# Kernel tuning notes

Measured on AMD Instinct MI355X. Metric: run time of the kernel, lower is better.

The kernel has to match this reference:

```python
import jax, jax.numpy as jnp
import numpy as np

NUM_HEADS = 12
EPS = 1e-6


def setup_inputs() -> dict:
    key = jax.random.key(0)
    k1, k2, k3, k4 = jax.random.split(key, 4)
    N, B, D = 1025, 8, 768
    x = jax.random.normal(k1, (N, B, D), dtype=jnp.float32)
    # torch nn.Linear weights: [out_features, in_features]
    w_qkv = jax.random.normal(k2, (3 * D, D), dtype=jnp.float32) * (D ** -0.5)
    w_proj = jax.random.normal(k3, (D, D), dtype=jnp.float32) * (D ** -0.5)
    b_proj = jax.random.normal(k4, (D,), dtype=jnp.float32) * 0.01
    return {"x": x, "w_qkv": w_qkv, "w_proj": w_proj, "b_proj": b_proj}


def reference(x, w_qkv, w_proj, b_proj):
    N, B, D = x.shape
    H = NUM_HEADS
    hd = D // H
    scale = hd ** -0.5
    scale_vv = scale * 1.0  # scale_multiplier = 1.0

    xb = jnp.transpose(x, (1, 0, 2))  # [B, N, D]
    qkv = xb @ w_qkv.T  # [B, N, 3D]
    qkv = qkv.reshape(B, N, 3, H, hd).transpose(2, 0, 3, 1, 4)  # [3, B, H, N, hd]
    q, k, v = qkv[0], qkv[1], qkv[2]

    # QK path: only row 0 of out_ori survives the masking, compute just that row
    scores0 = jnp.einsum('bhqd,bhkd->bhqk', q[:, :, :1], k) * scale  # [B,H,1,N]
    attn0 = jax.nn.softmax(scores0, axis=-1)
    out0 = jnp.einsum('bhqk,bhkd->bhqd', attn0, v)  # [B,H,1,hd]

    # VV cosine path: only rows 1: survive
    vn = v / jnp.maximum(jnp.linalg.norm(v, axis=-1, keepdims=True), EPS)
    scores_vv = jnp.einsum('bhqd,bhkd->bhqk', vn[:, :, 1:], vn) * scale_vv  # [B,H,N-1,N]
    attn_vv = jax.nn.softmax(scores_vv, axis=-1)
    out_vv = jnp.einsum('bhqk,bhkd->bhqd', attn_vv, v)  # [B,H,N-1,hd]

    out = jnp.concatenate([out0, out_vv], axis=2)  # [B,H,N,hd]
    out = out.transpose(0, 2, 1, 3).reshape(B, N, D)
    out = out @ w_proj.T + b_proj
    return jnp.transpose(out, (1, 0, 2))  # [N, B, D]
```

## Files before the change

### kernel.cpp

```cpp
#include <hip/hip_runtime.h>

typedef unsigned short u16;
typedef unsigned int   u32;
typedef __attribute__((ext_vector_type(8))) short short8;
typedef __attribute__((ext_vector_type(4))) float f32x4;

#define AS1 __attribute__((address_space(1)))
#define AS3 __attribute__((address_space(3)))

#define NSEQ  1025
#define BB    8
#define DD    768
#define HH    12
#define MROWS 8200
#define MPAD  8320
#define KPAD  1088

__device__ __forceinline__ void gl2lds16(const void* g, void* l) {
  __builtin_amdgcn_global_load_lds((const AS1 u32*)g, (AS3 u32*)l, 16, 0, 0);
}
__device__ __forceinline__ u16 f2bf(float f) {
  u32 u = __float_as_uint(f);
  return (u16)((u + 0x7FFFu + ((u >> 16) & 1u)) >> 16);
}
__device__ __forceinline__ float bf2f(u16 u) { return __uint_as_float(((u32)u) << 16); }

__global__ __launch_bounds__(256) void prep(const float* __restrict__ x,
                                            const float* __restrict__ wqkv,
                                            const float* __restrict__ wproj,
                                            u16* __restrict__ xb,
                                            u16* __restrict__ wkv,
                                            u16* __restrict__ wpj) {
  const int XB_G  = MPAD * 192;
  const int WKV_G = 1536 * 192;
  const int WPJ_G = 768 * 192;
  int g = blockIdx.x * 256 + threadIdx.x;
  float4 v;
  u16* dst;
  size_t di;
  if (g < XB_G) {
    int m = g / 192, e4 = g - m * 192;
    if (m < MROWS) {
      int bb = m / NSEQ, ns = m - bb * NSEQ;
      v = ((const float4*)x)[(size_t)(ns * BB + bb) * 192 + e4];
    } else {
      v.x = v.y = v.z = v.w = 0.f;
    }
    dst = xb; di = (size_t)g;
  } else if (g < XB_G + WKV_G) {
    int r = g - XB_G;
    v = ((const float4*)wqkv)[(size_t)147456 + r];
    dst = wkv; di = (size_t)r;
  } else if (g < XB_G + WKV_G + WPJ_G) {
    int r = g - XB_G - WKV_G;
    v = ((const float4*)wproj)[r];
    dst = wpj; di = (size_t)r;
  } else {
    return;
  }
  uint2 o;
  o.x = (u32)f2bf(v.x) | ((u32)f2bf(v.y) << 16);
  o.y = (u32)f2bf(v.z) | ((u32)f2bf(v.w) << 16);
  ((uint2*)dst)[di] = o;
}

template <int MODE, int NT>
__global__ __launch_bounds__(256) void gemm_bt(const u16* __restrict__ A,
                                               const u16* __restrict__ W,
                                               u16* __restrict__ Cbf,
                                               float* __restrict__ Cf,
                                               const float* __restrict__ bias,
                                               int ldc) {
  __shared__ u16 sA[128 * 64];
  __shared__ u16 sW[128 * 64];
  const int id = blockIdx.x;
  const int rx = id & 7, qx = id >> 3;
  const int kq = qx / NT;
  const int m_t = rx + (kq << 3);
  if (m_t > 64) return;
  const int n_t = qx - kq * NT;
  const int m0 = m_t << 7, n0 = n_t << 7;

  const int tid = threadIdx.x;
  const int w = tid >> 6, lane = tid & 63;
  const int wm = w & 1, wn = w >> 1;
  const int lc = lane & 15, lr = lane >> 4;

  f32x4 zero4 = {0.f, 0.f, 0.f, 0.f};
  f32x4 acc[4][4];
#pragma unroll
  for (int i = 0; i < 4; ++i)
#pragma unroll
    for (int j = 0; j < 4; ++j) acc[i][j] = zero4;

  const int r0 = tid >> 3;
  const int ko = (tid & 7) << 3;
  const u16* gA = A + (size_t)(m0 + r0) * DD + ko;
  const u16* gW = W + (size_t)(n0 + r0) * DD + ko;
  char* lA = (char*)sA + tid * 16;
  char* lW = (char*)sW + tid * 16;

#pragma unroll 1
  for (int kt = 0; kt < 12; ++kt) {
    __syncthreads();
#pragma unroll
    for (int j = 0; j < 4; ++j) {
      gl2lds16(gA + (size_t)j * 32 * DD + kt * 64, lA + j * 4096);
      gl2lds16(gW + (size_t)j * 32 * DD + kt * 64, lW + j * 4096);
    }
    __syncthreads();
#pragma unroll
    for (int kk = 0; kk < 2; ++kk) {
      short8 af[4], wf[4];
#pragma unroll
      for (int mt = 0; mt < 4; ++mt)
        af[mt] = *(const short8*)((char*)sA + ((wm << 6) + (mt << 4) + lc) * 128 + (kk << 6) + (lr << 4));
#pragma unroll
      for (int nt = 0; nt < 4; ++nt)
        wf[nt] = *(const short8*)((char*)sW + ((wn << 6) + (nt << 4) + lc) * 128 + (kk << 6) + (lr << 4));
#pragma unroll
      for (int mt = 0; mt < 4; ++mt)
#pragma unroll
        for (int nt = 0; nt < 4; ++nt)
          acc[mt][nt] = __builtin_amdgcn_mfma_f32_16x16x32_bf16(af[mt], wf[nt], acc[mt][nt], 0, 0, 0);
    }
  }

  if (MODE == 0) {
#pragma unroll
    for (int mt = 0; mt < 4; ++mt)
#pragma unroll
      for (int r = 0; r < 4; ++r) {
        int m = m0 + (wm << 6) + (mt << 4) + (lr << 2) + r;
        if (m < MROWS) {
          size_t base = (size_t)m * ldc + n0 + (wn << 6) + lc;
#pragma unroll
          for (int nt = 0; nt < 4; ++nt) Cbf[base + (nt << 4)] = f2bf(acc[mt][nt][r]);
        }
      }
  } else {
    float b4[4];
#pragma unroll
    for (int nt = 0; nt < 4; ++nt) b4[nt] = bias[n0 + (wn << 6) + (nt << 4) + lc];
#pragma unroll
    for (int mt = 0; mt < 4; ++mt)
#pragma unroll
      for (int r = 0; r < 4; ++r) {
        int m = m0 + (wm << 6) + (mt << 4) + (lr << 2) + r;
        if (m < MROWS) {
          int bb = m / NSEQ;
          int ns = m - bb * NSEQ;
          float* o = Cf + (size_t)ns * (BB * DD) + bb * DD + n0 + (wn << 6) + lc;
#pragma unroll
          for (int nt = 0; nt < 4; ++nt) o[nt << 4] = acc[mt][nt][r] + b4[nt];
        }
      }
  }
}

__global__ __launch_bounds__(256) void gemm_proj(const u16* __restrict__ A,
                                                 const u16* __restrict__ W,
                                                 float* __restrict__ Cf,
                                                 const float* __restrict__ bias) {
  __shared__ u16 sA[128 * 64];
  __shared__ u16 sW[64 * 64];
  const int id = blockIdx.x;
  const int rx = id & 7, qx = id >> 3;
  const int kq = qx / 12;
  const int m_t = rx + (kq << 3);
  if (m_t > 64) return;
  const int n_t = qx - kq * 12;
  const int m0 = m_t << 7, n0 = n_t << 6;

  const int tid = threadIdx.x;
  const int w = tid >> 6, lane = tid & 63;
  const int lc = lane & 15, lr = lane >> 4;

  f32x4 zero4 = {0.f, 0.f, 0.f, 0.f};
  f32x4 acc[2][4];
#pragma unroll
  for (int i = 0; i < 2; ++i)
#pragma unroll
    for (int j = 0; j < 4; ++j) acc[i][j] = zero4;

  const int r0 = tid >> 3;
  const int ko = (tid & 7) << 3;
  const u16* gA = A + (size_t)(m0 + r0) * DD + ko;
  const u16* gW = W + (size_t)(n0 + r0) * DD + ko;
  char* lA = (char*)sA + tid * 16;
  char* lW = (char*)sW + tid * 16;

#pragma unroll 1
  for (int kt = 0; kt < 12; ++kt) {
    __syncthreads();
#pragma unroll
    for (int j = 0; j < 4; ++j)
      gl2lds16(gA + (size_t)j * 32 * DD + kt * 64, lA + j * 4096);
#pragma unroll
    for (int j = 0; j < 2; ++j)
      gl2lds16(gW + (size_t)j * 32 * DD + kt * 64, lW + j * 4096);
    __syncthreads();
#pragma unroll
    for (int kk = 0; kk < 2; ++kk) {
      short8 af[2], wf[4];
#pragma unroll
      for (int mt = 0; mt < 2; ++mt)
        af[mt] = *(const short8*)((char*)sA + ((w << 5) + (mt << 4) + lc) * 128 + (kk << 6) + (lr << 4));
#pragma unroll
      for (int nt = 0; nt < 4; ++nt)
        wf[nt] = *(const short8*)((char*)sW + (((nt << 4) + lc) << 7) + (kk << 6) + (lr << 4));
#pragma unroll
      for (int mt = 0; mt < 2; ++mt)
#pragma unroll
        for (int nt = 0; nt < 4; ++nt)
          acc[mt][nt] = __builtin_amdgcn_mfma_f32_16x16x32_bf16(af[mt], wf[nt], acc[mt][nt], 0, 0, 0);
    }
  }

  float b4[4];
#pragma unroll
  for (int nt = 0; nt < 4; ++nt) b4[nt] = bias[n0 + (nt << 4) + lc];
#pragma unroll
  for (int mt = 0; mt < 2; ++mt)
#pragma unroll
    for (int r = 0; r < 4; ++r) {
      int m = m0 + (w << 5) + (mt << 4) + (lr << 2) + r;
      if (m < MROWS) {
        int bb = m / NSEQ;
        int ns = m - bb * NSEQ;
        float* o = Cf + (size_t)ns * (BB * DD) + bb * DD + n0 + lc;
#pragma unroll
        for (int nt = 0; nt < 4; ++nt) o[nt << 4] = acc[mt][nt][r] + b4[nt];
      }
    }
}

__global__ __launch_bounds__(256) void q0_kernel(const float* __restrict__ x,
                                                 const float* __restrict__ wq,
                                                 float* __restrict__ q0) {
  __shared__ float red[256];
  int bid = blockIdx.x;
  int b = bid / HH, c = bid - b * HH;
  int tid = threadIdx.x;
  int dp = (c << 6) + (tid >> 2), part = tid & 3;
  const float4* x4 = (const float4*)(x + (size_t)b * DD + part * 192);
  const float4* w4 = (const float4*)(wq + (size_t)dp * DD + part * 192);
  float acc = 0.f;
#pragma unroll 4
  for (int e = 0; e < 48; ++e) {
    float4 a = x4[e], w = w4[e];
    acc += a.x * w.x + a.y * w.y + a.z * w.z + a.w * w.w;
  }
  red[tid] = acc;
  __syncthreads();
  if (part == 0) q0[b * DD + dp] = red[tid] + red[tid + 1] + red[tid + 2] + red[tid + 3];
}

__global__ __launch_bounds__(256) void transpose_v(const u16* __restrict__ kv,
                                                   u16* __restrict__ vT,
                                                   u16* __restrict__ vn) {
  __shared__ u16 tile[64][72];
  __shared__ float red[256];
  __shared__ float sInv[64];
  int bid = blockIdx.x;
  int kc = bid % 17;
  int t2 = bid / 17;
  int h = t2 % HH, b = t2 / HH;
  int tid = threadIdx.x;
  int kl = tid >> 2, dc = (tid & 3) << 4;
  int key = kc * 64 + kl;
  u32 vals[8];
  if (key < NSEQ) {
    const u32* g = (const u32*)(kv + ((size_t)b * NSEQ + key) * 1536 + DD + h * 64 + dc);
#pragma unroll
    for (int i = 0; i < 8; ++i) vals[i] = g[i];
  } else {
#pragma unroll
    for (int i = 0; i < 8; ++i) vals[i] = 0;
  }
  float part = 0.f;
#pragma unroll
  for (int i = 0; i < 8; ++i) {
    float a = bf2f((u16)(vals[i] & 0xFFFF));
    float c = bf2f((u16)(vals[i] >> 16));
    part += a * a + c * c;
    ((u32*)&tile[kl][dc])[i] = vals[i];
  }
  red[tid] = part;
  __syncthreads();
  if ((tid & 3) == 0) {
    float s = red[tid] + red[tid + 1] + red[tid + 2] + red[tid + 3];
    sInv[kl] = (key < NSEQ) ? 1.0f / fmaxf(sqrtf(s), 1e-6f) : 0.0f;
  }
  __syncthreads();
  float iv = sInv[kl];
  u32 ovn[8];
#pragma unroll
  for (int i = 0; i < 8; ++i) {
    float a = bf2f((u16)(vals[i] & 0xFFFF)) * iv;
    float c = bf2f((u16)(vals[i] >> 16)) * iv;
    ovn[i] = (u32)f2bf(a) | ((u32)f2bf(c) << 16);
  }
  u32* on = (u32*)(vn + ((size_t)(b * HH + h) * KPAD + key) * 64 + dc);
#pragma unroll
  for (int i = 0; i < 8; ++i) on[i] = ovn[i];
  int dl = tid >> 2, ks = (tid & 3) << 4;
  u32 ov[8];
#pragma unroll
  for (int i = 0; i < 8; ++i)
    ov[i] = (u32)tile[ks + 2 * i][dl] | ((u32)tile[ks + 2 * i + 1][dl] << 16);
  u16* o = vT + (size_t)(b * HH + h) * 64 * KPAD + (size_t)dl * KPAD + kc * 64 + ks;
#pragma unroll
  for (int i = 0; i < 8; ++i) ((u32*)o)[i] = ov[i];
}

__global__ __launch_bounds__(256) void row0_part(const float* __restrict__ q0,
                                                 const u16* __restrict__ kv,
                                                 float* __restrict__ part) {
  __shared__ float sq[64];
  __shared__ float sc[129];
  __shared__ float red[256];
  __shared__ float rpv[32][68];
  int bh = blockIdx.x, ck = blockIdx.y;
  int b = bh / HH, h = bh - b * HH;
  int tid = threadIdx.x;
  if (tid < 64) sq[tid] = q0[b * DD + h * 64 + tid];
  if (tid == 64) sc[128] = 0.f;
  __syncthreads();
  const int nk = (ck == 7) ? 129 : 128;
  if (tid < nk) {
    int n = ck * 128 + tid;
    const u32* kr = (const u32*)(kv + ((size_t)b * NSEQ + n) * 1536 + h * 64);
    float s = 0.f;
#pragma unroll
    for (int i = 0; i < 32; ++i) {
      u32 u = kr[i];
      s += bf2f((u16)(u & 0xFFFF)) * sq[2 * i] + bf2f((u16)(u >> 16)) * sq[2 * i + 1];
    }
    sc[tid] = __expf(s * 0.125f);
  }
  __syncthreads();
  float ds = (tid < nk) ? sc[tid] : 0.f;
  red[tid] = ds;
  __syncthreads();
  for (int st = 128; st > 0; st >>= 1) {
    if (tid < st) red[tid] += red[tid + st];
    __syncthreads();
  }
  int kp = tid >> 3, dc = (tid & 7) << 3;
  const u16* vb = kv + (size_t)b * NSEQ * 1536 + DD + h * 64 + dc;
  float acc[8];
#pragma unroll
  for (int i = 0; i < 8; ++i) acc[i] = 0.f;
#pragma unroll
  for (int j = 0; j < 4; ++j) {
    int kl = kp + (j << 5);
    uint4 v = *(const uint4*)(vb + (size_t)(ck * 128 + kl) * 1536);
    float p = sc[kl];
    acc[0] += p * bf2f((u16)(v.x & 0xFFFF));
    acc[1] += p * bf2f((u16)(v.x >> 16));
    acc[2] += p * bf2f((u16)(v.y & 0xFFFF));
    acc[3] += p * bf2f((u16)(v.y >> 16));
    acc[4] += p * bf2f((u16)(v.z & 0xFFFF));
    acc[5] += p * bf2f((u16)(v.z >> 16));
    acc[6] += p * bf2f((u16)(v.w & 0xFFFF));
    acc[7] += p * bf2f((u16)(v.w >> 16));
  }
  if (ck == 7 && kp == 0) {
    uint4 v = *(const uint4*)(vb + (size_t)1024 * 1536);
    float p = sc[128];
    acc[0] += p * bf2f((u16)(v.x & 0xFFFF));
    acc[1] += p * bf2f((u16)(v.x >> 16));
    acc[2] += p * bf2f((u16)(v.y & 0xFFFF));
    acc[3] += p * bf2f((u16)(v.y >> 16));
    acc[4] += p * bf2f((u16)(v.z & 0xFFFF));
    acc[5] += p * bf2f((u16)(v.z >> 16));
    acc[6] += p * bf2f((u16)(v.w & 0xFFFF));
    acc[7] += p * bf2f((u16)(v.w >> 16));
  }
#pragma unroll
  for (int i = 0; i < 8; ++i) rpv[kp][dc + i] = acc[i];
  __syncthreads();
  float* po = part + ((size_t)bh * 8 + ck) * 65;
  if (tid < 64) {
    float s = 0.f;
#pragma unroll
    for (int p = 0; p < 32; ++p) s += rpv[p][tid];
    po[tid] = s;
  }
  if (tid == 64) po[64] = red[0];
}

__global__ __launch_bounds__(256, 4) void vv_attn(const u16* __restrict__ vn,
                                                  const u16* __restrict__ vT,
                                                  u16* __restrict__ attn,
                                                  const float* __restrict__ part) {
  __shared__ u16 sK[4096];
  __shared__ u16 sV[4096];
  __shared__ u16 sP[8192];

  const int tid = threadIdx.x, w = tid >> 6, lane = tid & 63;
  const int lc = lane & 15, lr = lane >> 4;
  const int bh = blockIdx.x;
  const int m0 = blockIdx.y << 7;
  const int b = bh / HH, h = bh - b * HH;
  const char* nb = (const char*)(vn + (size_t)bh * KPAD * 64);
  const char* tb = (const char*)(vT + (size_t)bh * 64 * KPAD);

  short8 qreg[2][2];
#pragma unroll
  for (int kk = 0; kk < 2; ++kk)
#pragma unroll
    for (int nt = 0; nt < 2; ++nt)
      qreg[kk][nt] = *(const short8*)(nb +
          (size_t)(1 + m0 + (w << 5) + (nt << 4) + lc) * 128 + (kk << 6) + (lr << 4));

  const char* srcK[2];
  const char* srcV[2];
  int offKV[2];
#pragma unroll
  for (int j = 0; j < 2; ++j) {
    int lin = (w << 11) + (j << 10) + (lane << 4);
    int kk = lin >> 12, kg = (lin >> 10) & 3;
    int lr2 = (lin >> 8) & 3, lc2 = (lin >> 4) & 15;
    srcK[j] = nb + (size_t)((kg << 4) + lc2) * 128 + (kk << 6) + (lr2 << 4);
    srcV[j] = tb + (size_t)((kg << 4) + lc2) * (KPAD * 2) + (kk << 6) + (lr2 << 4);
    offKV[j] = lin;
  }

  f32x4 zero4 = {0.f, 0.f, 0.f, 0.f};
  f32x4 oacc[2][4];
  f32x4 dacc[2];
#pragma unroll
  for (int i = 0; i < 2; ++i) {
    dacc[i] = zero4;
#pragma unroll
    for (int j = 0; j < 4; ++j) oacc[i][j] = zero4;
  }
  short8 ones;
#pragma unroll
  for (int i = 0; i < 8; ++i) ones[i] = (short)0x3F80;

  const float CEXP = 0.1803368801111204f;

  const char* rdK = (const char*)sK + (lane << 4);
  const char* rdV = (const char*)sV + (lane << 4);
  const char* rdP = (const char*)sP + (w << 12) + (lane << 4);
  char* wrP = (char*)sP + (w << 12) + ((lr >> 1) << 8) + (lc << 4) + ((lr & 1) << 3);

#pragma unroll 1
  for (int kt = 0; kt < 17; ++kt) {
    __syncthreads();
#pragma unroll
    for (int j = 0; j < 2; ++j) {
      gl2lds16(srcK[j] + (size_t)kt * 8192, (char*)sK + offKV[j]);
      gl2lds16(srcV[j] + (size_t)kt * 128,  (char*)sV + offKV[j]);
    }
    __syncthreads();

    f32x4 sacc[4][2];
#pragma unroll
    for (int mt = 0; mt < 4; ++mt)
#pragma unroll
      for (int nt = 0; nt < 2; ++nt) sacc[mt][nt] = zero4;
#pragma unroll
    for (int kk = 0; kk < 2; ++kk) {
      short8 ak[4];
#pragma unroll
      for (int mt = 0; mt < 4; ++mt)
        ak[mt] = *(const short8*)(rdK + (kk << 12) + (mt << 10));
#pragma unroll
      for (int mt = 0; mt < 4; ++mt)
#pragma unroll
        for (int nt = 0; nt < 2; ++nt)
          sacc[mt][nt] = __builtin_amdgcn_mfma_f32_16x16x32_bf16(ak[mt], qreg[kk][nt], sacc[mt][nt], 0, 0, 0);
    }

#pragma unroll
    for (int mt = 0; mt < 4; ++mt) {
#pragma unroll
      for (int nt = 0; nt < 2; ++nt) {
        f32x4 s = sacc[mt][nt];
        u32 a0 = __float_as_uint(__builtin_amdgcn_exp2f(s[0] * CEXP)) + 0x8000u;
        u32 a1 = __float_as_uint(__builtin_amdgcn_exp2f(s[1] * CEXP)) + 0x8000u;
        u32 a2 = __float_as_uint(__builtin_amdgcn_exp2f(s[2] * CEXP)) + 0x8000u;
        u32 a3 = __float_as_uint(__builtin_amdgcn_exp2f(s[3] * CEXP)) + 0x8000u;
        uint2 pv;
        pv.x = __builtin_amdgcn_perm(a1, a0, 0x07060302u);
        pv.y = __builtin_amdgcn_perm(a3, a2, 0x07060302u);
        if (kt == 16) {
          pv.x = (mt == 0 && lr == 0) ? (pv.x & 0xFFFFu) : 0u;
          pv.y = 0u;
        }
        *(uint2*)(wrP + ((mt >> 1) << 11) + (nt << 10) + ((mt & 1) << 9)) = pv;
      }
    }
    __builtin_amdgcn_sched_barrier(0);
    asm volatile("" ::: "memory");

#pragma unroll
    for (int h2 = 0; h2 < 2; ++h2) {
      if (!(kt == 16 && h2 == 1)) {
        short8 ap[2], bv[4];
#pragma unroll
        for (int mt = 0; mt < 2; ++mt)
          ap[mt] = *(const short8*)(rdP + (h2 << 11) + (mt << 10));
#pragma unroll
        for (int nt = 0; nt < 4; ++nt)
          bv[nt] = *(const short8*)(rdV + (h2 << 12) + (nt << 10));
#pragma unroll
        for (int mt = 0; mt < 2; ++mt) {
#pragma unroll
          for (int nt = 0; nt < 4; ++nt)
            oacc[mt][nt] = __builtin_amdgcn_mfma_f32_16x16x32_bf16(ap[mt], bv[nt], oacc[mt][nt], 0, 0, 0);
          dacc[mt] = __builtin_amdgcn_mfma_f32_16x16x32_bf16(ap[mt], ones, dacc[mt], 0, 0, 0);
        }
      }
    }
  }

#pragma unroll
  for (int mt = 0; mt < 2; ++mt) {
#pragma unroll
    for (int r = 0; r < 4; ++r) {
      int q = (w << 5) + (mt << 4) + (lr << 2) + r;
      int nseq = 1 + m0 + q;
      float rdn = 1.0f / dacc[mt][r];
      size_t obase = ((size_t)b * NSEQ + nseq) * DD + h * 64 + lc;
#pragma unroll
      for (int nt = 0; nt < 4; ++nt) attn[obase + (nt << 4)] = f2bf(oacc[mt][nt][r] * rdn);
    }
  }

  if (blockIdx.y == 0 && tid < 64) {
    const float* pp = part + (size_t)bh * 8 * 65;
    float num = 0.f, den = 0.f;
#pragma unroll
    for (int c = 0; c < 8; ++c) {
      num += pp[c * 65 + tid];
      den += pp[c * 65 + 64];
    }
    attn[(size_t)b * NSEQ * DD + h * 64 + tid] = f2bf(num / den);
  }
}

extern "C" void kernel_launch(void* const* d_in, const int* in_sizes, int n_in,
                              void* d_out, int out_size, void* d_ws, size_t ws_size,
                              hipStream_t stream) {
  const float* x      = (const float*)d_in[0];
  const float* w_qkv  = (const float*)d_in[1];
  const float* w_proj = (const float*)d_in[2];
  const float* b_proj = (const float*)d_in[3];
  float* out = (float*)d_out;
  char* ws = (char*)d_ws;

  u16*   xb   = (u16*)(ws + 0);
  u16*   vT   = (u16*)(ws + 0);
  u16*   wkv  = (u16*)(ws + 13369344);
  float* r0p  = (float*)(ws + 13369344);
  u16*   wpj  = (u16*)(ws + 15728640);
  u16*   kvb  = (u16*)(ws + 16908288);
  float* q0   = (float*)(ws + 42467328);
  u16*   attn = (u16*)(ws + 42491904);
  u16*   vn   = (u16*)(ws + 55271424);

  prep<<<7968, 256, 0, stream>>>(x, w_qkv, w_proj, xb, wkv, wpj);
  gemm_bt<0, 12><<<864, 256, 0, stream>>>(xb, wkv, kvb, nullptr, nullptr, 1536);
  q0_kernel<<<96, 256, 0, stream>>>(x, w_qkv, q0);
  transpose_v<<<1632, 256, 0, stream>>>(kvb, vT, vn);
  row0_part<<<dim3(96, 8), 256, 0, stream>>>(q0, kvb, r0p);
  vv_attn<<<dim3(96, 8), 256, 0, stream>>>(vn, vT, attn, r0p);
  gemm_proj<<<864, 256, 0, stream>>>(attn, wpj, out, b_proj);
}
```

Baseline: 213.8 us.

## Switch VV attention to 32x32 MFMA and keep P in registers via permlane32 swap

Rewrites the vv_attn inner loop to use 32x32x16 bf16 MFMAs instead of 16x16x32. The exponentiated scores are repacked into the A-operand layout with v_permlane32_swap, so the shared-memory P buffer and its write/read round trip go away. The K/V staging layout and the output indexing are changed to match the new fragment layout. The larger f32x16 accumulators raise register pressure, so launch bounds drop from 4 to 3 blocks per SM, which may reduce occupancy.

```diff
diff --git a/kernel.cpp b/kernel.cpp
--- a/kernel.cpp
+++ b/kernel.cpp
@@ -4,6 +4,8 @@
 typedef unsigned int   u32;
 typedef __attribute__((ext_vector_type(8))) short short8;
 typedef __attribute__((ext_vector_type(4))) float f32x4;
+typedef __attribute__((ext_vector_type(16))) float f32x16;
+typedef __attribute__((ext_vector_type(2))) unsigned int u32x2;
 
 #define AS1 __attribute__((address_space(1)))
 #define AS3 __attribute__((address_space(3)))
@@ -24,6 +26,15 @@
   return (u16)((u + 0x7FFFu + ((u >> 16) & 1u)) >> 16);
 }
 __device__ __forceinline__ float bf2f(u16 u) { return __uint_as_float(((u32)u) << 16); }
+
+__device__ __forceinline__ u32x2 pl32swap(u32 x, u32 y) {
+#if __has_builtin(__builtin_amdgcn_permlane32_swap)
+  return __builtin_amdgcn_permlane32_swap(x, y, false, false);
+#else
+  asm volatile("v_permlane32_swap_b32 %0, %1" : "+v"(x), "+v"(y));
+  u32x2 r; r.x = x; r.y = y; return r;
+#endif
+}
 
 __global__ __launch_bounds__(256) void prep(const float* __restrict__ x,
                                             const float* __restrict__ wqkv,
@@ -391,52 +402,41 @@
   if (tid == 64) po[64] = red[0];
 }
 
-__global__ __launch_bounds__(256, 4) void vv_attn(const u16* __restrict__ vn,
+__global__ __launch_bounds__(256, 3) void vv_attn(const u16* __restrict__ vn,
                                                   const u16* __restrict__ vT,
                                                   u16* __restrict__ attn,
                                                   const float* __restrict__ part) {
   __shared__ u16 sK[4096];
   __shared__ u16 sV[4096];
-  __shared__ u16 sP[8192];
 
   const int tid = threadIdx.x, w = tid >> 6, lane = tid & 63;
-  const int lc = lane & 15, lr = lane >> 4;
+  const int l5 = lane >> 5;
   const int bh = blockIdx.x;
   const int m0 = blockIdx.y << 7;
   const int b = bh / HH, h = bh - b * HH;
   const char* nb = (const char*)(vn + (size_t)bh * KPAD * 64);
   const char* tb = (const char*)(vT + (size_t)bh * 64 * KPAD);
 
-  short8 qreg[2][2];
-#pragma unroll
-  for (int kk = 0; kk < 2; ++kk)
-#pragma unroll
-    for (int nt = 0; nt < 2; ++nt)
-      qreg[kk][nt] = *(const short8*)(nb +
-          (size_t)(1 + m0 + (w << 5) + (nt << 4) + lc) * 128 + (kk << 6) + (lr << 4));
+  short8 qreg[4];
+#pragma unroll
+  for (int ds = 0; ds < 4; ++ds)
+    qreg[ds] = *(const short8*)(nb +
+        (size_t)(1 + m0 + (w << 5) + (lane & 31)) * 128 + (ds << 5) + (l5 << 4));
 
   const char* srcK[2];
   const char* srcV[2];
   int offKV[2];
 #pragma unroll
   for (int j = 0; j < 2; ++j) {
-    int lin = (w << 11) + (j << 10) + (lane << 4);
-    int kk = lin >> 12, kg = (lin >> 10) & 3;
-    int lr2 = (lin >> 8) & 3, lc2 = (lin >> 4) & 15;
-    srcK[j] = nb + (size_t)((kg << 4) + lc2) * 128 + (kk << 6) + (lr2 << 4);
-    srcV[j] = tb + (size_t)((kg << 4) + lc2) * (KPAD * 2) + (kk << 6) + (lr2 << 4);
-    offKV[j] = lin;
-  }
-
-  f32x4 zero4 = {0.f, 0.f, 0.f, 0.f};
-  f32x4 oacc[2][4];
-  f32x4 dacc[2];
-#pragma unroll
-  for (int i = 0; i < 2; ++i) {
-    dacc[i] = zero4;
-#pragma unroll
-    for (int j = 0; j < 4; ++j) oacc[i][j] = zero4;
-  }
+    srcK[j] = nb + (size_t)((j << 5) + (lane & 31)) * 128 + (w << 5) + (l5 << 4);
+    srcV[j] = tb + (size_t)((j << 5) + (lane & 31)) * (KPAD * 2) + (w << 5) + (l5 << 4);
+    offKV[j] = (w << 11) + (j << 10) + (lane << 4);
+  }
+
+  f32x16 oacc[2];
+  f32x16 dacc;
+#pragma unroll
+  for (int i = 0; i < 16; ++i) { oacc[0][i] = 0.f; oacc[1][i] = 0.f; dacc[i] = 0.f; }
   short8 ones;
 #pragma unroll
   for (int i = 0; i < 8; ++i) ones[i] = (short)0x3F80;
@@ -445,8 +445,6 @@
 
   const char* rdK = (const char*)sK + (lane << 4);
   const char* rdV = (const char*)sV + (lane << 4);
-  const char* rdP = (const char*)sP + (w << 12) + (lane << 4);
-  char* wrP = (char*)sP + (w << 12) + ((lr >> 1) << 8) + (lc << 4) + ((lr & 1) << 3);
 
 #pragma unroll 1
   for (int kt = 0; kt < 17; ++kt) {
@@ -458,78 +456,60 @@
     }
     __syncthreads();
 
-    f32x4 sacc[4][2];
-#pragma unroll
-    for (int mt = 0; mt < 4; ++mt)
-#pragma unroll
-      for (int nt = 0; nt < 2; ++nt) sacc[mt][nt] = zero4;
-#pragma unroll
-    for (int kk = 0; kk < 2; ++kk) {
-      short8 ak[4];
-#pragma unroll
-      for (int mt = 0; mt < 4; ++mt)
-        ak[mt] = *(const short8*)(rdK + (kk << 12) + (mt << 10));
-#pragma unroll
-      for (int mt = 0; mt < 4; ++mt)
-#pragma unroll
-        for (int nt = 0; nt < 2; ++nt)
-          sacc[mt][nt] = __builtin_amdgcn_mfma_f32_16x16x32_bf16(ak[mt], qreg[kk][nt], sacc[mt][nt], 0, 0, 0);
-    }
-
-#pragma unroll
-    for (int mt = 0; mt < 4; ++mt) {
-#pragma unroll
-      for (int nt = 0; nt < 2; ++nt) {
-        f32x4 s = sacc[mt][nt];
-        u32 a0 = __float_as_uint(__builtin_amdgcn_exp2f(s[0] * CEXP)) + 0x8000u;
-        u32 a1 = __float_as_uint(__builtin_amdgcn_exp2f(s[1] * CEXP)) + 0x8000u;
-        u32 a2 = __float_as_uint(__builtin_amdgcn_exp2f(s[2] * CEXP)) + 0x8000u;
-        u32 a3 = __float_as_uint(__builtin_amdgcn_exp2f(s[3] * CEXP)) + 0x8000u;
-        uint2 pv;
-        pv.x = __builtin_amdgcn_perm(a1, a0, 0x07060302u);
-        pv.y = __builtin_amdgcn_perm(a3, a2, 0x07060302u);
+    f32x16 sacc[2];
+#pragma unroll
+    for (int i = 0; i < 16; ++i) { sacc[0][i] = 0.f; sacc[1][i] = 0.f; }
+#pragma unroll
+    for (int ds = 0; ds < 4; ++ds) {
+      short8 ak0 = *(const short8*)(rdK + ((ds << 1) << 10));
+      short8 ak1 = *(const short8*)(rdK + (((ds << 1) + 1) << 10));
+      sacc[0] = __builtin_amdgcn_mfma_f32_32x32x16_bf16(ak0, qreg[ds], sacc[0], 0, 0, 0);
+      sacc[1] = __builtin_amdgcn_mfma_f32_32x32x16_bf16(ak1, qreg[ds], sacc[1], 0, 0, 0);
+    }
+
+#pragma unroll
+    for (int mt = 0; mt < 2; ++mt) {
+      u32 pk[8];
+#pragma unroll
+      for (int i = 0; i < 8; ++i) {
+        float e0 = __builtin_amdgcn_exp2f(sacc[mt][2 * i] * CEXP);
+        float e1 = __builtin_amdgcn_exp2f(sacc[mt][2 * i + 1] * CEXP);
         if (kt == 16) {
-          pv.x = (mt == 0 && lr == 0) ? (pv.x & 0xFFFFu) : 0u;
-          pv.y = 0u;
+          e0 = (mt == 0 && i == 0 && l5 == 0) ? e0 : 0.f;
+          e1 = 0.f;
         }
-        *(uint2*)(wrP + ((mt >> 1) << 11) + (nt << 10) + ((mt & 1) << 9)) = pv;
+        pk[i] = __builtin_amdgcn_perm(__float_as_uint(e1) + 0x8000u,
+                                      __float_as_uint(e0) + 0x8000u, 0x07060302u);
       }
-    }
-    __builtin_amdgcn_sched_barrier(0);
-    asm volatile("" ::: "memory");
-
-#pragma unroll
-    for (int h2 = 0; h2 < 2; ++h2) {
-      if (!(kt == 16 && h2 == 1)) {
-        short8 ap[2], bv[4];
-#pragma unroll
-        for (int mt = 0; mt < 2; ++mt)
-          ap[mt] = *(const short8*)(rdP + (h2 << 11) + (mt << 10));
-#pragma unroll
-        for (int nt = 0; nt < 4; ++nt)
-          bv[nt] = *(const short8*)(rdV + (h2 << 12) + (nt << 10));
-#pragma unroll
-        for (int mt = 0; mt < 2; ++mt) {
-#pragma unroll
-          for (int nt = 0; nt < 4; ++nt)
-            oacc[mt][nt] = __builtin_amdgcn_mfma_f32_16x16x32_bf16(ap[mt], bv[nt], oacc[mt][nt], 0, 0, 0);
-          dacc[mt] = __builtin_amdgcn_mfma_f32_16x16x32_bf16(ap[mt], ones, dacc[mt], 0, 0, 0);
+#pragma unroll
+      for (int s = 0; s < 2; ++s) {
+        u32x2 r0 = pl32swap(pk[4 * s], pk[4 * s + 2]);
+        u32x2 r1 = pl32swap(pk[4 * s + 1], pk[4 * s + 3]);
+        u32 paw[4] = {r0.x, r1.x, r0.y, r1.y};
+        short8 pa;
+#pragma unroll
+        for (int q2 = 0; q2 < 4; ++q2) {
+          pa[2 * q2]     = (short)(paw[q2] & 0xFFFFu);
+          pa[2 * q2 + 1] = (short)(paw[q2] >> 16);
         }
+        int ksg = (mt << 1) + s;
+        short8 bv0 = *(const short8*)(rdV + ((ksg << 1) << 10));
+        short8 bv1 = *(const short8*)(rdV + (((ksg << 1) + 1) << 10));
+        oacc[0] = __builtin_amdgcn_mfma_f32_32x32x16_bf16(pa, bv0, oacc[0], 0, 0, 0);
+        oacc[1] = __builtin_amdgcn_mfma_f32_32x32x16_bf16(pa, bv1, oacc[1], 0, 0, 0);
+        dacc    = __builtin_amdgcn_mfma_f32_32x32x16_bf16(pa, ones, dacc, 0, 0, 0);
       }
     }
   }
 
 #pragma unroll
-  for (int mt = 0; mt < 2; ++mt) {
-#pragma unroll
-    for (int r = 0; r < 4; ++r) {
-      int q = (w << 5) + (mt << 4) + (lr << 2) + r;
-      int nseq = 1 + m0 + q;
-      float rdn = 1.0f / dacc[mt][r];
-      size_t obase = ((size_t)b * NSEQ + nseq) * DD + h * 64 + lc;
-#pragma unroll
-      for (int nt = 0; nt < 4; ++nt) attn[obase + (nt << 4)] = f2bf(oacc[mt][nt][r] * rdn);
-    }
+  for (int reg = 0; reg < 16; ++reg) {
+    int q = (reg & 3) + ((reg >> 2) << 3) + (l5 << 2);
+    int nseq = 1 + m0 + (w << 5) + q;
+    float rdn = 1.0f / dacc[reg];
+    u16* o = attn + ((size_t)b * NSEQ + nseq) * DD + h * 64 + (lane & 31);
+    o[0]  = f2bf(oacc[0][reg] * rdn);
+    o[32] = f2bf(oacc[1][reg] * rdn);
   }
 
   if (blockIdx.y == 0 && tid < 64) {
```

Result: no change. 214.4 us, median of 3 (+0.3%).
